# Optimization experiments

Measured on AMD Instinct MI355X. Metric: run time of the kernel, lower is better.

The kernel has to match this reference:

```python
import jax, jax.numpy as jnp
import numpy as np


def setup_inputs() -> dict:
    key = jax.random.key(0)
    k1, k2 = jax.random.split(key)
    B, N, M, D = 2, 8192, 8192, 3
    inp = {
        "input": jax.random.normal(k1, (B, N, D), dtype=jnp.float32),
        "point": jax.random.normal(k2, (B, M, D), dtype=jnp.float32),
    }
    return inp


def reference(input, point):
    # One-sided Chamfer: for each query point, squared distance to its
    # nearest neighbor in the reference cloud `input`.
    # ||p - q||^2 = |p|^2 + |q|^2 - 2 p.q  (expanded form avoids a [B,M,N,3] tensor)
    p2 = jnp.sum(point * point, axis=-1)               # [B, M]
    q2 = jnp.sum(input * input, axis=-1)               # [B, N]
    cross = jnp.einsum("bmd,bnd->bmn", point, input)   # [B, M, N]
    d2 = p2[:, :, None] + q2[:, None, :] - 2.0 * cross
    d2 = jnp.maximum(d2, 0.0)
    return jnp.min(d2, axis=-1)                        # [B, M]
```

## Files before the change

### kernel.cpp

```cpp
#include <hip/hip_runtime.h>


typedef __attribute__((ext_vector_type(8)))  short  short8;
typedef __attribute__((ext_vector_type(16))) float  f32x16;

constexpr int BB = 2;
constexpr int NN = 8192;
constexpr int MM = 8192;
constexpr int BM = BB * MM;

constexpr int QB = 128;
constexpr int NS = 8;
constexpr int SL = NN / NS;
constexpr int NT = SL / 32;

__device__ inline unsigned short f2bf(float f) {
    unsigned u = __float_as_uint(f);
    return (unsigned short)((u + 0x7FFFu + ((u >> 16) & 1u)) >> 16);
}
__device__ inline float bf2f(unsigned short h) {
    return __uint_as_float((unsigned)h << 16);
}

__global__ __launch_bounds__(256) void chamfer_mfma_kernel(
    const float* __restrict__ input,
    const float* __restrict__ point,
    float* __restrict__ ws)
{
    __shared__ short8 frag[NT * 64];

    const int tid  = threadIdx.x;
    const int lane = tid & 63;
    const int w    = tid >> 6;
    const int b    = blockIdx.z;
    const int qb0  = blockIdx.x * QB;
    const int n0   = blockIdx.y * SL;

    const float* inb = input + (size_t)b * NN * 3;
    for (int e = tid; e < NT * 64; e += 256) {
        const int t = e >> 6, l = e & 63;
        const int n = n0 + t * 32 + (l & 31);
        const float x = inb[n * 3 + 0];
        const float y = inb[n * 3 + 1];
        const float z = inb[n * 3 + 2];
        const float q2 = fmaf(z, z, fmaf(y, y, x * x));
        const unsigned short hx = f2bf(x), hy = f2bf(y), hz = f2bf(z);
        const unsigned short lx = f2bf(x - bf2f(hx));
        const unsigned short ly = f2bf(y - bf2f(hy));
        const unsigned short lz = f2bf(z - bf2f(hz));
        const unsigned short q2h = f2bf(q2);
        const unsigned short q2l = f2bf(q2 - bf2f(q2h));
        short8 v;
        if ((l >> 5) == 0) {
            v[0] = (short)hx; v[1] = (short)hy; v[2] = (short)hz; v[3] = (short)hx;
            v[4] = (short)hy; v[5] = (short)hz; v[6] = (short)lx; v[7] = (short)ly;
        } else {
            v[0] = (short)lz; v[1] = (short)q2h; v[2] = (short)q2l; v[3] = 0;
            v[4] = 0; v[5] = 0; v[6] = 0; v[7] = 0;
        }
        frag[e] = v;
    }

    const int col = lane & 31, h = lane >> 5;
    const int m   = qb0 + w * 32 + col;
    const float* pp = point + ((size_t)b * MM + m) * 3;
    const float x = pp[0], y = pp[1], z = pp[2];
    const float p2 = fmaf(z, z, fmaf(y, y, x * x));
    const float hxf = bf2f(f2bf(x)), hyf = bf2f(f2bf(y)), hzf = bf2f(f2bf(z));
    const unsigned short bhx = f2bf(-2.0f * hxf);
    const unsigned short bhy = f2bf(-2.0f * hyf);
    const unsigned short bhz = f2bf(-2.0f * hzf);
    const unsigned short blx = f2bf(-2.0f * (x - hxf));
    const unsigned short bly = f2bf(-2.0f * (y - hyf));
    const unsigned short blz = f2bf(-2.0f * (z - hzf));
    const short one = (short)0x3F80;
    short8 bq;
    if (h == 0) {
        bq[0] = (short)bhx; bq[1] = (short)bhy; bq[2] = (short)bhz; bq[3] = (short)blx;
        bq[4] = (short)bly; bq[5] = (short)blz; bq[6] = (short)bhx; bq[7] = (short)bhy;
    } else {
        bq[0] = (short)bhz; bq[1] = one; bq[2] = one; bq[3] = 0;
        bq[4] = 0; bq[5] = 0; bq[6] = 0; bq[7] = 0;
    }

    __syncthreads();

    f32x16 zero;
#pragma unroll
    for (int i = 0; i < 16; ++i) zero[i] = 0.0f;
    float tmin = 3.0e38f;

#pragma unroll 2
    for (int t = 0; t < NT; ++t) {
        const short8 af = frag[t * 64 + lane];
        const f32x16 d = __builtin_amdgcn_mfma_f32_32x32x16_bf16(af, bq, zero, 0, 0, 0);
        const float m0 = fminf(fminf(d[0],  d[1]),  d[2]);
        const float m1 = fminf(fminf(d[3],  d[4]),  d[5]);
        const float m2 = fminf(fminf(d[6],  d[7]),  d[8]);
        const float m3 = fminf(fminf(d[9],  d[10]), d[11]);
        const float m4 = fminf(fminf(d[12], d[13]), d[14]);
        const float r0 = fminf(fminf(m0, m1), d[15]);
        const float r1 = fminf(fminf(m2, m3), m4);
        tmin = fminf(fminf(tmin, r0), r1);
    }

    tmin = fminf(tmin, __shfl_xor(tmin, 32, 64));
    if (h == 0) {
        float* wsy = ws + (size_t)blockIdx.y * BM + (size_t)b * MM;
        wsy[m] = fmaxf(tmin + p2, 0.0f);
    }
}

__global__ __launch_bounds__(256) void chamfer_reduce_kernel(
    const float* __restrict__ ws, float* __restrict__ out)
{
    const int o = blockIdx.x * 256 + threadIdx.x;
    float acc = ws[o];
#pragma unroll
    for (int y = 1; y < NS; ++y)
        acc = fminf(acc, ws[(size_t)y * BM + o]);
    out[o] = acc;
}

extern "C" void kernel_launch(void* const* d_in, const int* in_sizes, int n_in,
                              void* d_out, int out_size, void* d_ws, size_t ws_size,
                              hipStream_t stream) {
    const float* input = (const float*)d_in[0];
    const float* point = (const float*)d_in[1];
    float* out = (float*)d_out;
    float* ws  = (float*)d_ws;

    dim3 grid1(MM / QB, NS, BB);
    chamfer_mfma_kernel<<<grid1, dim3(256), 0, stream>>>(input, point, ws);

    chamfer_reduce_kernel<<<dim3(BM / 256), dim3(256), 0, stream>>>(ws, out);
}
```

Measured before the change: 16.52 us.

## Precompute input fragments once in a prep kernel and reduce per block

Moves the bf16 split-fragment construction for the reference cloud into its own prep kernel that writes to workspace, so the fragments are no longer rebuilt in every block. The main kernel now gives each block 32 queries and 8 waves, each wave scanning a slice of N with fragments read from global/L2 instead of LDS. The per-wave minima are combined in shared memory, which removes the separate reduce kernel. In exchange, every fragment load now goes to global memory instead of LDS, and the launch bound now targets 512-thread blocks.

```diff
diff --git a/kernel.cpp b/kernel.cpp
--- a/kernel.cpp
+++ b/kernel.cpp
@@ -7,12 +7,11 @@
 constexpr int BB = 2;
 constexpr int NN = 8192;
 constexpr int MM = 8192;
-constexpr int BM = BB * MM;
 
-constexpr int QB = 128;
-constexpr int NS = 8;
-constexpr int SL = NN / NS;
-constexpr int NT = SL / 32;
+constexpr int TILES = NN / 32;
+constexpr int WPB   = 8;
+constexpr int TPW   = TILES / WPB;
+constexpr int BQ    = WPB * 64;
 
 __device__ inline unsigned short f2bf(float f) {
     unsigned u = __float_as_uint(f);
@@ -22,47 +21,53 @@
     return __uint_as_float((unsigned)h << 16);
 }
 
-__global__ __launch_bounds__(256) void chamfer_mfma_kernel(
+__global__ __launch_bounds__(256) void chamfer_prep_kernel(
     const float* __restrict__ input,
+    short8* __restrict__ frag)
+{
+    const int e = blockIdx.x * 256 + threadIdx.x;
+    const int b = e >> 14;
+    const int r = e & 16383;
+    const int t = r >> 6, l = r & 63;
+    const int n = t * 32 + (l & 31);
+
+    const float* inb = input + (size_t)b * NN * 3;
+    const float x = inb[n * 3 + 0];
+    const float y = inb[n * 3 + 1];
+    const float z = inb[n * 3 + 2];
+    const float q2 = fmaf(z, z, fmaf(y, y, x * x));
+    const unsigned short hx = f2bf(x), hy = f2bf(y), hz = f2bf(z);
+    const unsigned short lx = f2bf(x - bf2f(hx));
+    const unsigned short ly = f2bf(y - bf2f(hy));
+    const unsigned short lz = f2bf(z - bf2f(hz));
+    const unsigned short q2h = f2bf(q2);
+    const unsigned short q2l = f2bf(q2 - bf2f(q2h));
+    short8 v;
+    if ((l >> 5) == 0) {
+        v[0] = (short)hx; v[1] = (short)hy; v[2] = (short)hz; v[3] = (short)hx;
+        v[4] = (short)hy; v[5] = (short)hz; v[6] = (short)lx; v[7] = (short)ly;
+    } else {
+        v[0] = (short)lz; v[1] = (short)q2h; v[2] = (short)q2l; v[3] = 0;
+        v[4] = 0; v[5] = 0; v[6] = 0; v[7] = 0;
+    }
+    frag[e] = v;
+}
+
+__global__ __launch_bounds__(BQ, 4) void chamfer_main_kernel(
+    const short8* __restrict__ frag,
     const float* __restrict__ point,
-    float* __restrict__ ws)
+    float* __restrict__ out)
 {
-    __shared__ short8 frag[NT * 64];
+    __shared__ float pm[WPB][32];
 
     const int tid  = threadIdx.x;
     const int lane = tid & 63;
     const int w    = tid >> 6;
-    const int b    = blockIdx.z;
-    const int qb0  = blockIdx.x * QB;
-    const int n0   = blockIdx.y * SL;
-
-    const float* inb = input + (size_t)b * NN * 3;
-    for (int e = tid; e < NT * 64; e += 256) {
-        const int t = e >> 6, l = e & 63;
-        const int n = n0 + t * 32 + (l & 31);
-        const float x = inb[n * 3 + 0];
-        const float y = inb[n * 3 + 1];
-        const float z = inb[n * 3 + 2];
-        const float q2 = fmaf(z, z, fmaf(y, y, x * x));
-        const unsigned short hx = f2bf(x), hy = f2bf(y), hz = f2bf(z);
-        const unsigned short lx = f2bf(x - bf2f(hx));
-        const unsigned short ly = f2bf(y - bf2f(hy));
-        const unsigned short lz = f2bf(z - bf2f(hz));
-        const unsigned short q2h = f2bf(q2);
-        const unsigned short q2l = f2bf(q2 - bf2f(q2h));
-        short8 v;
-        if ((l >> 5) == 0) {
-            v[0] = (short)hx; v[1] = (short)hy; v[2] = (short)hz; v[3] = (short)hx;
-            v[4] = (short)hy; v[5] = (short)hz; v[6] = (short)lx; v[7] = (short)ly;
-        } else {
-            v[0] = (short)lz; v[1] = (short)q2h; v[2] = (short)q2l; v[3] = 0;
-            v[4] = 0; v[5] = 0; v[6] = 0; v[7] = 0;
-        }
-        frag[e] = v;
-    }
+    const int b    = blockIdx.y;
+    const int qb0  = blockIdx.x * 32;
 
     const int col = lane & 31, h = lane >> 5;
-    const int m   = qb0 + w * 32 + col;
+    const int m   = qb0 + col;
     const float* pp = point + ((size_t)b * MM + m) * 3;
     const float x = pp[0], y = pp[1], z = pp[2];
     const float p2 = fmaf(z, z, fmaf(y, y, x * x));
@@ -83,16 +88,15 @@
         bq[4] = 0; bq[5] = 0; bq[6] = 0; bq[7] = 0;
     }
 
-    __syncthreads();
-
     f32x16 zero;
 #pragma unroll
     for (int i = 0; i < 16; ++i) zero[i] = 0.0f;
     float tmin = 3.0e38f;
 
-#pragma unroll 2
-    for (int t = 0; t < NT; ++t) {
-        const short8 af = frag[t * 64 + lane];
+    const short8* fw = frag + (size_t)b * (TILES * 64) + (size_t)w * TPW * 64;
+#pragma unroll 4
+    for (int t = 0; t < TPW; ++t) {
+        const short8 af = fw[t * 64 + lane];
         const f32x16 d = __builtin_amdgcn_mfma_f32_32x32x16_bf16(af, bq, zero, 0, 0, 0);
         const float m0 = fminf(fminf(d[0],  d[1]),  d[2]);
         const float m1 = fminf(fminf(d[3],  d[4]),  d[5]);
@@ -105,21 +109,14 @@
     }
 
     tmin = fminf(tmin, __shfl_xor(tmin, 32, 64));
-    if (h == 0) {
-        float* wsy = ws + (size_t)blockIdx.y * BM + (size_t)b * MM;
-        wsy[m] = fmaxf(tmin + p2, 0.0f);
+    if (h == 0) pm[w][col] = tmin;
+    __syncthreads();
+    if (w == 0 && h == 0) {
+        float v = pm[0][col];
+#pragma unroll
+        for (int r = 1; r < WPB; ++r) v = fminf(v, pm[r][col]);
+        out[(size_t)b * MM + m] = fmaxf(v + p2, 0.0f);
     }
-}
-
-__global__ __launch_bounds__(256) void chamfer_reduce_kernel(
-    const float* __restrict__ ws, float* __restrict__ out)
-{
-    const int o = blockIdx.x * 256 + threadIdx.x;
-    float acc = ws[o];
-#pragma unroll
-    for (int y = 1; y < NS; ++y)
-        acc = fminf(acc, ws[(size_t)y * BM + o]);
-    out[o] = acc;
 }
 
 extern "C" void kernel_launch(void* const* d_in, const int* in_sizes, int n_in,
@@ -127,11 +124,11 @@
                               hipStream_t stream) {
     const float* input = (const float*)d_in[0];
     const float* point = (const float*)d_in[1];
-    float* out = (float*)d_out;
-    float* ws  = (float*)d_ws;
+    float* out   = (float*)d_out;
+    short8* frag = (short8*)d_ws;
 
-    dim3 grid1(MM / QB, NS, BB);
-    chamfer_mfma_kernel<<<grid1, dim3(256), 0, stream>>>(input, point, ws);
+    chamfer_prep_kernel<<<dim3(BB * TILES * 64 / 256), dim3(256), 0, stream>>>(input, frag);
 
-    chamfer_reduce_kernel<<<dim3(BM / 256), dim3(256), 0, stream>>>(ws, out);
+    dim3 grid(MM / 32, BB);
+    chamfer_main_kernel<<<grid, dim3(BQ), 0, stream>>>(frag, point, out);
 }
```

Result: slower. 17.16 us (+3.9%).
